# Optimization experiments

Measured on AMD Instinct MI355X. Metric: run time of the kernel, lower is better.

Reference implementation:

```python
import jax, jax.numpy as jnp
import numpy as np


def _gru_scan(x_seq, Wih, Whh, bih, bhh):
    # x_seq: (S, N, D); PyTorch GRU/GRUCell gate math, h0 = 0. Returns (S, N, H).
    H = Whh.shape[1]
    gi_all = x_seq @ Wih.T + bih  # precompute input projections: (S, N, 3H)

    def step(h, gi):
        gh = h @ Whh.T + bhh
        ir, iz, inn = jnp.split(gi, 3, axis=-1)
        hr, hz, hn = jnp.split(gh, 3, axis=-1)
        r = jax.nn.sigmoid(ir + hr)
        z = jax.nn.sigmoid(iz + hz)
        n = jnp.tanh(inn + r * hn)
        h_new = (1.0 - z) * n + z * h
        return h_new, h_new

    h0 = jnp.zeros((x_seq.shape[1], H), x_seq.dtype)
    _, ys = jax.lax.scan(step, h0, gi_all)
    return ys


def setup_inputs() -> dict:
    key = jax.random.key(0)
    ks = jax.random.split(key, 40)
    B, T = 32, 800
    NOTE, E, P, H0, H1, FE, RE = 128, 256, 256, 512, 512, 64, 64

    def w(k, shape):
        return jax.random.normal(k, shape, dtype=jnp.float32) * 0.05

    return {
        "note": jax.random.randint(ks[0], (B, T), 0, NOTE, dtype=jnp.int64),
        "f0_prev": jax.random.normal(ks[1], (B, T), dtype=jnp.float32),
        "rmse_prev": jax.random.normal(ks[2], (B, T), dtype=jnp.float32),
        "note_emb": w(ks[3], (NOTE, E)),
        "f0_W": w(ks[4], (FE, 1)), "f0_b": w(ks[5], (FE,)),
        "rmse_W": w(ks[6], (RE, 1)), "rmse_b": w(ks[7], (RE,)),
        "pre1_W": w(ks[8], (P, E)), "pre1_b": w(ks[9], (P,)),
        "pre2_W": w(ks[10], (P, P)), "pre2_b": w(ks[11], (P,)),
        "encf_Wih": w(ks[12], (3 * H0, P)), "encf_Whh": w(ks[13], (3 * H0, H0)),
        "encf_bih": w(ks[14], (3 * H0,)), "encf_bhh": w(ks[15], (3 * H0,)),
        "encb_Wih": w(ks[16], (3 * H0, P)), "encb_Whh": w(ks[17], (3 * H0, H0)),
        "encb_bih": w(ks[18], (3 * H0,)), "encb_bhh": w(ks[19], (3 * H0,)),
        "decf_Wih": w(ks[20], (3 * H1, 2 * H0 + FE)), "decf_Whh": w(ks[21], (3 * H1, H1)),
        "decf_bih": w(ks[22], (3 * H1,)), "decf_bhh": w(ks[23], (3 * H1,)),
        "decr_Wih": w(ks[24], (3 * H1, 2 * H0 + RE)), "decr_Whh": w(ks[25], (3 * H1, H1)),
        "decr_bih": w(ks[26], (3 * H1,)), "decr_bhh": w(ks[27], (3 * H1,)),
        "postf_W": w(ks[28], (1, H1)), "postf_b": w(ks[29], (1,)),
        "postr_W": w(ks[30], (1, H1)), "postr_b": w(ks[31], (1,)),
    }


def reference(note, f0_prev, rmse_prev, note_emb, f0_W, f0_b, rmse_W, rmse_b,
              pre1_W, pre1_b, pre2_W, pre2_b,
              encf_Wih, encf_Whh, encf_bih, encf_bhh,
              encb_Wih, encb_Whh, encb_bih, encb_bhh,
              decf_Wih, decf_Whh, decf_bih, decf_bhh,
              decr_Wih, decr_Whh, decr_bih, decr_bhh,
              postf_W, postf_b, postr_W, postr_b):
    # Embeddings. Linear(1, FE) on a [B,T] signal == outer-broadcast with W[:,0].
    ne = note_emb[note]                                   # (B, T, E)
    f0e = f0_prev[..., None] * f0_W[:, 0] + f0_b          # (B, T, FE)
    rme = rmse_prev[..., None] * rmse_W[:, 0] + rmse_b    # (B, T, RE)

    # Prenet: Linear -> Tanh -> Linear -> Tanh
    h = jnp.tanh(jnp.tanh(ne @ pre1_W.T + pre1_b) @ pre2_W.T + pre2_b)  # (B, T, P)

    # Encoder: torch nn.GRU built WITHOUT batch_first and called with lengths=None,
    # so the recurrence runs over axis 0 (B) with T acting as the GRU batch. Replicated.
    ef = _gru_scan(h, encf_Wih, encf_Whh, encf_bih, encf_bhh)            # (B, T, H0)
    eb = _gru_scan(h[::-1], encb_Wih, encb_Whh, encb_bih, encb_bhh)[::-1]
    enc = jnp.concatenate([ef, eb], axis=-1)                             # (B, T, 2H0)

    # Decoders: GRUCell loop over T with teacher forcing (y_prevs has T>1 steps),
    # so step-t input is concat(enc[:, t], embed(prev[:, t])) -> standard scan.
    xt = jnp.transpose(enc, (1, 0, 2))                                   # (T, B, 2H0)
    hf = _gru_scan(jnp.concatenate([xt, jnp.transpose(f0e, (1, 0, 2))], -1),
                   decf_Wih, decf_Whh, decf_bih, decf_bhh)               # (T, B, H1)
    hr = _gru_scan(jnp.concatenate([xt, jnp.transpose(rme, (1, 0, 2))], -1),
                   decr_Wih, decr_Whh, decr_bih, decr_bhh)               # (T, B, H1)

    f0 = jnp.transpose((hf @ postf_W.T + postf_b)[..., 0], (1, 0))       # (B, T)
    rmse = jnp.transpose((hr @ postr_W.T + postr_b)[..., 0], (1, 0))     # (B, T)
    return (f0, rmse)
```

## Files before the change

kernel.cpp:

```cpp
#include <hip/hip_runtime.h>
#include <hip/hip_bf16.h>


typedef __bf16 bf16;
typedef bf16 bf16x8 __attribute__((ext_vector_type(8)));
typedef float f32x4 __attribute__((ext_vector_type(4)));

#define BATCH 32
#define TLEN 800
#define BT (BATCH * TLEN)

__device__ __forceinline__ float bf2f(bf16 v) {
    unsigned short u = __builtin_bit_cast(unsigned short, v);
    unsigned int x = ((unsigned int)u) << 16;
    return __builtin_bit_cast(float, x);
}
__device__ __forceinline__ bf16 f2bf(float f) {
    unsigned int x = __builtin_bit_cast(unsigned int, f);
    unsigned int r = (x + 0x7FFFu + ((x >> 16) & 1u)) >> 16;
    return __builtin_bit_cast(bf16, (unsigned short)r);
}
__device__ __forceinline__ bf16x8 ld8f(const float* p) {
    f32x4 a = *(const f32x4*)p;
    f32x4 b = *(const f32x4*)(p + 4);
    bf16x8 r;
#pragma unroll
    for (int i = 0; i < 4; i++) {
        r[i] = f2bf(a[i]);
        r[i + 4] = f2bf(b[i]);
    }
    return r;
}
__device__ __forceinline__ void splitv(f32x4 a, f32x4 b, bf16x8& vh, bf16x8& vl) {
#pragma unroll
    for (int j = 0; j < 4; j++) {
        bf16 h0 = f2bf(a[j]);
        vh[j] = h0;
        vl[j] = f2bf(a[j] - bf2f(h0));
        bf16 h1 = f2bf(b[j]);
        vh[j + 4] = h1;
        vl[j + 4] = f2bf(b[j] - bf2f(h1));
    }
}
__device__ __forceinline__ f32x4 mfma16(bf16x8 a, bf16x8 b, f32x4 c) {
    return __builtin_amdgcn_mfma_f32_16x16x32_bf16(a, b, c, 0, 0, 0);
}
__device__ __forceinline__ float sigm(float x) { return 1.f / (1.f + __expf(-x)); }

template <int MODE>
__global__ __launch_bounds__(256) void gemm01_k(
    const int* __restrict__ note, const float* __restrict__ asrc,
    const float* __restrict__ W, const float* __restrict__ bias,
    float* __restrict__ out, int t0, int TC) {
    __shared__ bf16 Ah[128][72], Al[128][72], Bs[128][72];

    const int tid = threadIdx.x;
    const int lane = tid & 63, wv = tid >> 6;
    const int wm = wv & 1, wn = wv >> 1;
    const int l15 = lane & 15, hi = lane >> 4;
    const int bm = blockIdx.x * 128, bn = blockIdx.y * 128;
    const int ch = (tid & 7) * 8, arow = tid >> 3;

    f32x4 acc[4][4] = {};
    const float* ap[4];
    if (MODE == 0) {
        int zc = 0;
        for (int i = 0; i < 64; i++) zc += (note[2 * i + 1] == 0) ? 1 : 0;
        const bool n64 = (zc >= 60);
#pragma unroll
        for (int i = 0; i < 4; i++) {
            int m = bm + arow + 32 * i;
            int b = m / TC, tt = m - b * TC;
            int idx = b * TLEN + t0 + tt;
            int id = n64 ? note[2 * idx] : note[idx];
            id = id < 0 ? 0 : (id > 127 ? 127 : id);
            ap[i] = asrc + (size_t)id * 256;
        }
    } else {
#pragma unroll
        for (int i = 0; i < 4; i++) ap[i] = asrc + (size_t)(bm + arow + 32 * i) * 256;
    }

    for (int k0 = 0; k0 < 256; k0 += 64) {
#pragma unroll
        for (int i = 0; i < 4; i++) {
            int row = arow + 32 * i;
            f32x4 va = *(const f32x4*)(ap[i] + k0 + ch);
            f32x4 vb = *(const f32x4*)(ap[i] + k0 + ch + 4);
            bf16x8 vh, vl;
            splitv(va, vb, vh, vl);
            *(bf16x8*)&Ah[row][ch] = vh;
            *(bf16x8*)&Al[row][ch] = vl;
        }
#pragma unroll
        for (int i = 0; i < 4; i++) {
            int row = arow + 32 * i;
            *(bf16x8*)&Bs[row][ch] = ld8f(W + (size_t)(bn + row) * 256 + k0 + ch);
        }
        __syncthreads();
#pragma unroll
        for (int kk = 0; kk < 64; kk += 32) {
            bf16x8 ah[4], al[4], bb[4];
#pragma unroll
            for (int mt = 0; mt < 4; mt++) {
                ah[mt] = *(const bf16x8*)&Ah[wm * 64 + mt * 16 + l15][kk + hi * 8];
                al[mt] = *(const bf16x8*)&Al[wm * 64 + mt * 16 + l15][kk + hi * 8];
            }
#pragma unroll
            for (int nt = 0; nt < 4; nt++)
                bb[nt] = *(const bf16x8*)&Bs[wn * 64 + nt * 16 + l15][kk + hi * 8];
#pragma unroll
            for (int mt = 0; mt < 4; mt++)
#pragma unroll
                for (int nt = 0; nt < 4; nt++) {
                    acc[mt][nt] = mfma16(ah[mt], bb[nt], acc[mt][nt]);
                    acc[mt][nt] = mfma16(al[mt], bb[nt], acc[mt][nt]);
                }
        }
        __syncthreads();
    }

#pragma unroll
    for (int mt = 0; mt < 4; mt++)
#pragma unroll
        for (int nt = 0; nt < 4; nt++) {
            int n = bn + wn * 64 + nt * 16 + l15;
            float bs = bias[n];
#pragma unroll
            for (int r = 0; r < 4; r++) {
                int m = bm + wm * 64 + mt * 16 + hi * 4 + r;
                out[(size_t)m * 256 + n] = tanhf(acc[mt][nt][r] + bs);
            }
        }
}

__global__ __launch_bounds__(256) void gemm2_k(
    const float* __restrict__ ef, const float* __restrict__ eb,
    const float* __restrict__ sig, const float* __restrict__ sigW,
    const float* __restrict__ sigB, const float* __restrict__ W,
    const float* __restrict__ bias, float* __restrict__ out, int t0, int TC) {
    __shared__ bf16 Ah[128][72], Al[128][72];
    __shared__ bf16 Bh[64][72], Bl[64][72];

    const int tid = threadIdx.x;
    const int lane = tid & 63, wv = tid >> 6;
    const int wm = wv & 1, wn = wv >> 1;
    const int l15 = lane & 15, hi = lane >> 4;
    const int bm = blockIdx.x * 128, bn = blockIdx.y * 64;
    const int ch = (tid & 7) * 8, arow = tid >> 3;

    f32x4 acc[4][2] = {};
    int rb[4];
    float sigv[4];
#pragma unroll
    for (int i = 0; i < 4; i++) {
        int m = bm + arow + 32 * i;
        int tt = m >> 5, b = m & 31;
        rb[i] = b * TC + tt;
        sigv[i] = sig[b * TLEN + t0 + tt];
    }

    for (int k0 = 0; k0 < 1088; k0 += 64) {
#pragma unroll
        for (int i = 0; i < 4; i++) {
            int row = arow + 32 * i;
            int k = k0 + ch;
            f32x4 va, vb;
            if (k < 512) {
                va = *(const f32x4*)(ef + (size_t)rb[i] * 512 + k);
                vb = *(const f32x4*)(ef + (size_t)rb[i] * 512 + k + 4);
            } else if (k < 1024) {
                va = *(const f32x4*)(eb + (size_t)rb[i] * 512 + (k - 512));
                vb = *(const f32x4*)(eb + (size_t)rb[i] * 512 + (k - 512) + 4);
            } else {
                f32x4 w0 = *(const f32x4*)(sigW + ch);
                f32x4 w1 = *(const f32x4*)(sigW + ch + 4);
                f32x4 b0 = *(const f32x4*)(sigB + ch);
                f32x4 b1 = *(const f32x4*)(sigB + ch + 4);
                float s = sigv[i];
#pragma unroll
                for (int j = 0; j < 4; j++) {
                    va[j] = s * w0[j] + b0[j];
                    vb[j] = s * w1[j] + b1[j];
                }
            }
            bf16x8 vh, vl;
            splitv(va, vb, vh, vl);
            *(bf16x8*)&Ah[row][ch] = vh;
            *(bf16x8*)&Al[row][ch] = vl;
        }
#pragma unroll
        for (int i = 0; i < 2; i++) {
            int row = arow + 32 * i;
            const float* src = W + (size_t)(bn + row) * 1088 + k0 + ch;
            f32x4 va = *(const f32x4*)src;
            f32x4 vb = *(const f32x4*)(src + 4);
            bf16x8 vh, vl;
            splitv(va, vb, vh, vl);
            *(bf16x8*)&Bh[row][ch] = vh;
            *(bf16x8*)&Bl[row][ch] = vl;
        }
        __syncthreads();
#pragma unroll
        for (int kk = 0; kk < 64; kk += 32) {
            bf16x8 ah[4], al[4], bh[2], bl[2];
#pragma unroll
            for (int mt = 0; mt < 4; mt++) {
                ah[mt] = *(const bf16x8*)&Ah[wm * 64 + mt * 16 + l15][kk + hi * 8];
                al[mt] = *(const bf16x8*)&Al[wm * 64 + mt * 16 + l15][kk + hi * 8];
            }
#pragma unroll
            for (int nt = 0; nt < 2; nt++) {
                bh[nt] = *(const bf16x8*)&Bh[wn * 32 + nt * 16 + l15][kk + hi * 8];
                bl[nt] = *(const bf16x8*)&Bl[wn * 32 + nt * 16 + l15][kk + hi * 8];
            }
#pragma unroll
            for (int mt = 0; mt < 4; mt++)
#pragma unroll
                for (int nt = 0; nt < 2; nt++) {
                    acc[mt][nt] = mfma16(ah[mt], bh[nt], acc[mt][nt]);
                    acc[mt][nt] = mfma16(al[mt], bh[nt], acc[mt][nt]);
                    acc[mt][nt] = mfma16(ah[mt], bl[nt], acc[mt][nt]);
                }
        }
        __syncthreads();
    }

#pragma unroll
    for (int mt = 0; mt < 4; mt++)
#pragma unroll
        for (int nt = 0; nt < 2; nt++) {
            int n = bn + wn * 32 + nt * 16 + l15;
            float bs = bias[n];
#pragma unroll
            for (int r = 0; r < 4; r++) {
                int m = bm + wm * 64 + mt * 16 + hi * 4 + r;
                out[(size_t)m * 1536 + n] = acc[mt][nt][r] + bs;
            }
        }
}

__global__ __launch_bounds__(256) void enc_step_k(
    int step, int TC, const float* __restrict__ hpre, float* __restrict__ efb,
    float* __restrict__ ebb, const float* __restrict__ fWih,
    const float* __restrict__ fWhh, const float* __restrict__ fbih,
    const float* __restrict__ fbhh, const float* __restrict__ bWih,
    const float* __restrict__ bWhh, const float* __restrict__ bbih,
    const float* __restrict__ bbhh) {
    __shared__ bf16 As[32][72], Alo[32][72];
    __shared__ bf16 Bs[96][72], Blo[96][72];

    const int dir = blockIdx.z;
    const float* Wih = dir ? bWih : fWih;
    const float* Whh = dir ? bWhh : fWhh;
    const float* bih = dir ? bbih : fbih;
    const float* bhh = dir ? bbhh : fbhh;
    float* outb = dir ? ebb : efb;
    const int bsrc = dir ? (31 - step) : step;
    const int prevb = dir ? (32 - step) : (step - 1);

    const int tid = threadIdx.x;
    const int lane = tid & 63, wv = tid >> 6;
    const int mt = wv & 1, jt = wv >> 1;
    const int l15 = lane & 15, hi = lane >> 4;
    const int mtile = blockIdx.x, jtile = blockIdx.y;
    const int ch = (tid & 7) * 8, arow = tid >> 3;

    f32x4 acc_r = {}, acc_z = {}, acc_in = {}, acc_hn = {};

    const int nblocks = (step == 0) ? 4 : 12;
    for (int kb = 0; kb < nblocks; kb++) {
        int k0 = kb * 64;
        {
            int trow = mtile * 32 + arow;
            int tcl = trow < TC ? trow : TC - 1;
            const float* src = (k0 < 256)
                                   ? (hpre + ((size_t)bsrc * TC + tcl) * 256 + k0 + ch)
                                   : (outb + ((size_t)prevb * TC + tcl) * 512 + (k0 - 256) + ch);
            f32x4 va = *(const f32x4*)src;
            f32x4 vb = *(const f32x4*)(src + 4);
            bf16x8 vh, vl;
            splitv(va, vb, vh, vl);
            *(bf16x8*)&As[arow][ch] = vh;
            *(bf16x8*)&Alo[arow][ch] = vl;
        }
#pragma unroll
        for (int i = 0; i < 3; i++) {
            int row = arow + 32 * i;
            int s = row >> 5, j = row & 31;
            int wr = s * 512 + jtile * 32 + j;
            const float* src = (k0 < 256) ? (Wih + (size_t)wr * 256 + k0 + ch)
                                          : (Whh + (size_t)wr * 512 + (k0 - 256) + ch);
            f32x4 va = *(const f32x4*)src;
            f32x4 vb = *(const f32x4*)(src + 4);
            bf16x8 vh, vl;
            splitv(va, vb, vh, vl);
            *(bf16x8*)&Bs[row][ch] = vh;
            *(bf16x8*)&Blo[row][ch] = vl;
        }
        __syncthreads();
#pragma unroll
        for (int kk = 0; kk < 64; kk += 32) {
            bf16x8 a = *(const bf16x8*)&As[mt * 16 + l15][kk + hi * 8];
            bf16x8 alo = *(const bf16x8*)&Alo[mt * 16 + l15][kk + hi * 8];
            bf16x8 brh = *(const bf16x8*)&Bs[jt * 16 + l15][kk + hi * 8];
            bf16x8 brl = *(const bf16x8*)&Blo[jt * 16 + l15][kk + hi * 8];
            bf16x8 bzh = *(const bf16x8*)&Bs[32 + jt * 16 + l15][kk + hi * 8];
            bf16x8 bzl = *(const bf16x8*)&Blo[32 + jt * 16 + l15][kk + hi * 8];
            bf16x8 bnh = *(const bf16x8*)&Bs[64 + jt * 16 + l15][kk + hi * 8];
            bf16x8 bnl = *(const bf16x8*)&Blo[64 + jt * 16 + l15][kk + hi * 8];
            acc_r = mfma16(a, brh, acc_r);
            acc_r = mfma16(alo, brh, acc_r);
            acc_r = mfma16(a, brl, acc_r);
            acc_z = mfma16(a, bzh, acc_z);
            acc_z = mfma16(alo, bzh, acc_z);
            acc_z = mfma16(a, bzl, acc_z);
            if (k0 < 256) {
                acc_in = mfma16(a, bnh, acc_in);
                acc_in = mfma16(alo, bnh, acc_in);
                acc_in = mfma16(a, bnl, acc_in);
            } else {
                acc_hn = mfma16(a, bnh, acc_hn);
                acc_hn = mfma16(alo, bnh, acc_hn);
                acc_hn = mfma16(a, bnl, acc_hn);
            }
        }
        __syncthreads();
    }

    int j = jtile * 32 + jt * 16 + l15;
    float bir = bih[j] + bhh[j];
    float biz = bih[512 + j] + bhh[512 + j];
    float bin = bih[1024 + j];
    float bhn = bhh[1024 + j];
#pragma unroll
    for (int r = 0; r < 4; r++) {
        int trow = mtile * 32 + mt * 16 + hi * 4 + r;
        if (trow < TC) {
            float rr = sigm(acc_r[r] + bir);
            float zz = sigm(acc_z[r] + biz);
            float nn = tanhf(acc_in[r] + bin + rr * (acc_hn[r] + bhn));
            float hp = (step > 0) ? outb[((size_t)prevb * TC + trow) * 512 + j] : 0.f;
            outb[((size_t)bsrc * TC + trow) * 512 + j] = (1.f - zz) * nn + zz * hp;
        }
    }
}

__global__ __launch_bounds__(256, 1) void dec_k(
    const float* __restrict__ giF, const float* __restrict__ giR,
    const float* __restrict__ WhhF, const float* __restrict__ WhhR,
    const float* __restrict__ bhhF, const float* __restrict__ bhhR,
    float* __restrict__ HcurF, float* __restrict__ HcurR,
    const float* __restrict__ HprevF, const float* __restrict__ HprevR,
    int* __restrict__ flags, int t0, int TC) {
    const int d = blockIdx.x >> 4;
    const int g = blockIdx.x & 15;
    const float* gi = d ? giR : giF;
    const float* Whh = d ? WhhR : WhhF;
    const float* bhh = d ? bhhR : bhhF;
    float* Hcur = d ? HcurR : HcurF;
    const float* Hprev = d ? HprevR : HprevF;
    int* flg = flags + d * TLEN;

    const int tid = threadIdx.x;
    const int lane = tid & 63, wv = tid >> 6;
    const int mt = wv & 1, jt = wv >> 1;
    const int l15 = lane & 15, hi = lane >> 4;
    const int j_abs = g * 32 + jt * 16 + l15;

    bf16x8 Wf[3][16];
#pragma unroll
    for (int s = 0; s < 3; s++)
#pragma unroll
        for (int kb = 0; kb < 16; kb++)
            Wf[s][kb] = ld8f(Whh + (size_t)(s * 512 + j_abs) * 512 + kb * 32 + hi * 8);

    const float bhr = bhh[j_abs];
    const float bhz = bhh[512 + j_abs];
    const float bhn = bhh[1024 + j_abs];

    for (int tt = 0; tt < TC; tt++) {
        const int t = t0 + tt;
        float gr[4], gz[4], gn[4];
#pragma unroll
        for (int r = 0; r < 4; r++) {
            int b = mt * 16 + hi * 4 + r;
            const float* gp = gi + ((size_t)tt * BATCH + b) * 1536 + j_abs;
            gr[r] = gp[0];
            gz[r] = gp[512];
            gn[r] = gp[1024];
        }

        f32x4 ar = {}, az = {}, an = {};
        float hp[4] = {0.f, 0.f, 0.f, 0.f};
        if (t > 0) {
            const float* base;
            if (tt > 0) {
                if (tid == 0) {
                    while (__hip_atomic_load(&flg[t - 1], __ATOMIC_ACQUIRE,
                                             __HIP_MEMORY_SCOPE_AGENT) < 16)
                        __builtin_amdgcn_s_sleep(1);
                }
                __syncthreads();
                __threadfence();
                base = Hcur + (size_t)(tt - 1) * BATCH * 512;
            } else {
                base = Hprev + (size_t)(TC - 1) * BATCH * 512;
            }
            const float* ap = base + (size_t)(mt * 16 + l15) * 512 + hi * 8;
#pragma unroll
            for (int half = 0; half < 2; half++) {
                f32x4 raw[8][2];
#pragma unroll
                for (int q = 0; q < 8; q++) {
                    int kb = half * 8 + q;
                    raw[q][0] = *(const f32x4*)(ap + kb * 32);
                    raw[q][1] = *(const f32x4*)(ap + kb * 32 + 4);
                }
#pragma unroll
                for (int q = 0; q < 8; q++) {
                    int kb = half * 8 + q;
                    bf16x8 ah, al;
                    splitv(raw[q][0], raw[q][1], ah, al);
                    ar = mfma16(ah, Wf[0][kb], ar);
                    ar = mfma16(al, Wf[0][kb], ar);
                    az = mfma16(ah, Wf[1][kb], az);
                    az = mfma16(al, Wf[1][kb], az);
                    an = mfma16(ah, Wf[2][kb], an);
                    an = mfma16(al, Wf[2][kb], an);
                }
            }
#pragma unroll
            for (int r = 0; r < 4; r++) {
                int b = mt * 16 + hi * 4 + r;
                hp[r] = base[(size_t)b * 512 + j_abs];
            }
        }
#pragma unroll
        for (int r = 0; r < 4; r++) {
            int b = mt * 16 + hi * 4 + r;
            float rr = sigm(gr[r] + ar[r] + bhr);
            float zz = sigm(gz[r] + az[r] + bhz);
            float nn = tanhf(gn[r] + rr * (an[r] + bhn));
            Hcur[((size_t)tt * BATCH + b) * 512 + j_abs] = (1.f - zz) * nn + zz * hp[r];
        }
        __syncthreads();
        if (tid == 0)
            __hip_atomic_fetch_add(&flg[t], 1, __ATOMIC_RELEASE, __HIP_MEMORY_SCOPE_AGENT);
    }
}

__global__ __launch_bounds__(256) void post_k(
    const float* __restrict__ H, const float* __restrict__ W,
    const float* __restrict__ bs, float* __restrict__ out, int t0) {
    const int wv = threadIdx.x >> 6, lane = threadIdx.x & 63;
    const int row = blockIdx.x * 4 + wv;
    const int tt = row >> 5, b = row & 31;
    const float bias = bs[0];
    const float* hp = H + (size_t)row * 512 + lane * 8;
    f32x4 h0 = *(const f32x4*)hp;
    f32x4 h1 = *(const f32x4*)(hp + 4);
    f32x4 w0 = *(const f32x4*)(W + lane * 8);
    f32x4 w1 = *(const f32x4*)(W + lane * 8 + 4);
    float s = 0.f;
#pragma unroll
    for (int i = 0; i < 4; i++) s += h0[i] * w0[i] + h1[i] * w1[i];
#pragma unroll
    for (int off = 32; off > 0; off >>= 1) s += __shfl_down(s, off);
    if (lane == 0) out[b * TLEN + t0 + tt] = s + bias;
}

__global__ void zero_k(int* __restrict__ flags) {
    int i = blockIdx.x * 256 + threadIdx.x;
    if (i < 2 * TLEN) flags[i] = 0;
}

extern "C" void kernel_launch(void* const* d_in, const int* in_sizes, int n_in,
                              void* d_out, int out_size, void* d_ws, size_t ws_size,
                              hipStream_t stream) {
    const int* note = (const int*)d_in[0];
    const float* f0_prev = (const float*)d_in[1];
    const float* rmse_prev = (const float*)d_in[2];
    const float* note_emb = (const float*)d_in[3];
    const float* f0_W = (const float*)d_in[4];
    const float* f0_b = (const float*)d_in[5];
    const float* rmse_W = (const float*)d_in[6];
    const float* rmse_b = (const float*)d_in[7];
    const float* pre1_W = (const float*)d_in[8];
    const float* pre1_b = (const float*)d_in[9];
    const float* pre2_W = (const float*)d_in[10];
    const float* pre2_b = (const float*)d_in[11];
    const float* encf_Wih = (const float*)d_in[12];
    const float* encf_Whh = (const float*)d_in[13];
    const float* encf_bih = (const float*)d_in[14];
    const float* encf_bhh = (const float*)d_in[15];
    const float* encb_Wih = (const float*)d_in[16];
    const float* encb_Whh = (const float*)d_in[17];
    const float* encb_bih = (const float*)d_in[18];
    const float* encb_bhh = (const float*)d_in[19];
    const float* decf_Wih = (const float*)d_in[20];
    const float* decf_Whh = (const float*)d_in[21];
    const float* decf_bih = (const float*)d_in[22];
    const float* decf_bhh = (const float*)d_in[23];
    const float* decr_Wih = (const float*)d_in[24];
    const float* decr_Whh = (const float*)d_in[25];
    const float* decr_bih = (const float*)d_in[26];
    const float* decr_bhh = (const float*)d_in[27];
    const float* postf_W = (const float*)d_in[28];
    const float* postf_b = (const float*)d_in[29];
    const float* postr_W = (const float*)d_in[30];
    const float* postr_b = (const float*)d_in[31];
    float* out = (float*)d_out;

    const int tcs[9] = {800, 400, 200, 100, 80, 40, 20, 8, 4};
    int TC = 4;
    for (int i = 0; i < 9; i++) {
        int tc = tcs[i];
        int slots = (tc == TLEN) ? 1 : 2;
        size_t need = (size_t)(2 * 65536 + 2 * 196608 + 2 * slots * 65536) * tc + 65536;
        if (ws_size >= need) { TC = tc; break; }
    }
    const int NC = TLEN / TC;
    const int slots = (NC == 1) ? 1 : 2;

    char* ws = (char*)d_ws;
    size_t off = 0;
    auto carve = [&](size_t bytes) {
        void* p = ws + off;
        off += (bytes + 255) & ~(size_t)255;
        return p;
    };
    const size_t slotB = (size_t)65536 * TC;
    float* ef_c = (float*)carve(slotB);
    float* eb_c = (float*)carve(slotB);
    float* giF_c = (float*)carve((size_t)196608 * TC);
    float* giR_c = (float*)carve((size_t)196608 * TC);
    float* ringF = (float*)carve(slotB * slots);
    float* ringR = (float*)carve(slotB * slots);
    int* flags = (int*)carve(2 * TLEN * 4);
    float* t1_c = giF_c;
    float* hpre_c = giF_c + (size_t)8192 * TC;

    zero_k<<<dim3(7), 256, 0, stream>>>(flags);

    const size_t slotE = (size_t)TC * BATCH * 512;

    for (int c = 0; c < NC; c++) {
        const int t0 = c * TC;
        const int mg = TC * 32 / 128;

        gemm01_k<0><<<dim3(mg, 2), 256, 0, stream>>>(note, note_emb, pre1_W, pre1_b,
                                                     t1_c, t0, TC);
        gemm01_k<1><<<dim3(mg, 2), 256, 0, stream>>>(nullptr, t1_c, pre2_W, pre2_b,
                                                     hpre_c, t0, TC);
        const int etiles = (TC + 31) / 32;
        for (int i = 0; i < 32; i++)
            enc_step_k<<<dim3(etiles, 16, 2), 256, 0, stream>>>(
                i, TC, hpre_c, ef_c, eb_c, encf_Wih, encf_Whh, encf_bih, encf_bhh,
                encb_Wih, encb_Whh, encb_bih, encb_bhh);

        gemm2_k<<<dim3(mg, 24), 256, 0, stream>>>(ef_c, eb_c, f0_prev, f0_W, f0_b,
                                                  decf_Wih, decf_bih, giF_c, t0, TC);
        gemm2_k<<<dim3(mg, 24), 256, 0, stream>>>(ef_c, eb_c, rmse_prev, rmse_W,
                                                  rmse_b, decr_Wih, decr_bih, giR_c,
                                                  t0, TC);

        float* HcurF = ringF + (size_t)(c & (slots - 1)) * slotE;
        const float* HprevF = ringF + (size_t)((c - 1) & (slots - 1)) * slotE;
        float* HcurR = ringR + (size_t)(c & (slots - 1)) * slotE;
        const float* HprevR = ringR + (size_t)((c - 1) & (slots - 1)) * slotE;

        dec_k<<<dim3(32), 256, 0, stream>>>(giF_c, giR_c, decf_Whh, decr_Whh,
                                            decf_bhh, decr_bhh, HcurF, HcurR,
                                            HprevF, HprevR, flags, t0, TC);

        post_k<<<dim3(TC * 32 / 4), 256, 0, stream>>>(HcurF, postf_W, postf_b,
                                                      out, t0);
        post_k<<<dim3(TC * 32 / 4), 256, 0, stream>>>(HcurR, postr_W, postr_b,
                                                      out + BT, t0);
    }
    (void)in_sizes; (void)n_in; (void)out_size; (void)ws_size;
}
```

Measured before the change: 13.19 ms.

## Replace per-step counter barrier with per-block progress flags and relaxed coherent loads

The decoder's cross-block barrier changes from one atomic counter per timestep to one progress flag per block. Each block stores t+1 into its own flag, and 16 lanes of wave 0 poll all the flags in parallel. The acquire/release semantics and the explicit threadfence are dropped. Hidden-state stores and loads become relaxed agent-scope atomics, and the block's own previous h is kept in registers instead of being reloaded. The aim is to cut the latency of the per-step synchronisation in the serial 800-step recurrence. The cost is that correctness now relies on relaxed ordering behaving well on this hardware.

```diff
diff --git a/kernel.cpp b/kernel.cpp
--- a/kernel.cpp
+++ b/kernel.cpp
@@ -5,6 +5,7 @@
 typedef __bf16 bf16;
 typedef bf16 bf16x8 __attribute__((ext_vector_type(8)));
 typedef float f32x4 __attribute__((ext_vector_type(4)));
+typedef float f32x2 __attribute__((ext_vector_type(2)));
 
 #define BATCH 32
 #define TLEN 800
@@ -46,6 +47,29 @@
     return __builtin_amdgcn_mfma_f32_16x16x32_bf16(a, b, c, 0, 0, 0);
 }
 __device__ __forceinline__ float sigm(float x) { return 1.f / (1.f + __expf(-x)); }
+
+__device__ __forceinline__ void cst_f32(float* p, float v) {
+    __hip_atomic_store((unsigned int*)p, __builtin_bit_cast(unsigned int, v),
+                       __ATOMIC_RELAXED, __HIP_MEMORY_SCOPE_AGENT);
+}
+__device__ __forceinline__ float cld_f32(const float* p) {
+    unsigned int u = __hip_atomic_load((const unsigned int*)p, __ATOMIC_RELAXED,
+                                       __HIP_MEMORY_SCOPE_AGENT);
+    return __builtin_bit_cast(float, u);
+}
+__device__ __forceinline__ f32x4 cld_f32x4(const float* p) {
+    unsigned long long a = __hip_atomic_load((const unsigned long long*)p,
+                                             __ATOMIC_RELAXED,
+                                             __HIP_MEMORY_SCOPE_AGENT);
+    unsigned long long b = __hip_atomic_load((const unsigned long long*)(p + 2),
+                                             __ATOMIC_RELAXED,
+                                             __HIP_MEMORY_SCOPE_AGENT);
+    f32x2 fa = __builtin_bit_cast(f32x2, a);
+    f32x2 fb = __builtin_bit_cast(f32x2, b);
+    f32x4 r;
+    r[0] = fa[0]; r[1] = fa[1]; r[2] = fb[0]; r[3] = fb[1];
+    return r;
+}
 
 template <int MODE>
 __global__ __launch_bounds__(256) void gemm01_k(
@@ -360,7 +384,7 @@
     const float* bhh = d ? bhhR : bhhF;
     float* Hcur = d ? HcurR : HcurF;
     const float* Hprev = d ? HprevR : HprevF;
-    int* flg = flags + d * TLEN;
+    int* flg = flags + d * 16;
 
     const int tid = threadIdx.x;
     const int lane = tid & 63, wv = tid >> 6;
@@ -378,6 +402,8 @@
     const float bhr = bhh[j_abs];
     const float bhz = bhh[512 + j_abs];
     const float bhn = bhh[1024 + j_abs];
+
+    float hpreg[4] = {0.f, 0.f, 0.f, 0.f};
 
     for (int tt = 0; tt < TC; tt++) {
         const int t = t0 + tt;
@@ -396,13 +422,12 @@
         if (t > 0) {
             const float* base;
             if (tt > 0) {
-                if (tid == 0) {
-                    while (__hip_atomic_load(&flg[t - 1], __ATOMIC_ACQUIRE,
-                                             __HIP_MEMORY_SCOPE_AGENT) < 16)
+                if (wv == 0 && lane < 16) {
+                    while (__hip_atomic_load(&flg[lane], __ATOMIC_RELAXED,
+                                             __HIP_MEMORY_SCOPE_AGENT) < t)
                         __builtin_amdgcn_s_sleep(1);
                 }
                 __syncthreads();
-                __threadfence();
                 base = Hcur + (size_t)(tt - 1) * BATCH * 512;
             } else {
                 base = Hprev + (size_t)(TC - 1) * BATCH * 512;
@@ -414,8 +439,8 @@
 #pragma unroll
                 for (int q = 0; q < 8; q++) {
                     int kb = half * 8 + q;
-                    raw[q][0] = *(const f32x4*)(ap + kb * 32);
-                    raw[q][1] = *(const f32x4*)(ap + kb * 32 + 4);
+                    raw[q][0] = cld_f32x4(ap + kb * 32);
+                    raw[q][1] = cld_f32x4(ap + kb * 32 + 4);
                 }
 #pragma unroll
                 for (int q = 0; q < 8; q++) {
@@ -430,10 +455,15 @@
                     an = mfma16(al, Wf[2][kb], an);
                 }
             }
-#pragma unroll
-            for (int r = 0; r < 4; r++) {
-                int b = mt * 16 + hi * 4 + r;
-                hp[r] = base[(size_t)b * 512 + j_abs];
+            if (tt > 0) {
+#pragma unroll
+                for (int r = 0; r < 4; r++) hp[r] = hpreg[r];
+            } else {
+#pragma unroll
+                for (int r = 0; r < 4; r++) {
+                    int b = mt * 16 + hi * 4 + r;
+                    hp[r] = cld_f32(base + (size_t)b * 512 + j_abs);
+                }
             }
         }
 #pragma unroll
@@ -442,11 +472,14 @@
             float rr = sigm(gr[r] + ar[r] + bhr);
             float zz = sigm(gz[r] + az[r] + bhz);
             float nn = tanhf(gn[r] + rr * (an[r] + bhn));
-            Hcur[((size_t)tt * BATCH + b) * 512 + j_abs] = (1.f - zz) * nn + zz * hp[r];
+            float hnew = (1.f - zz) * nn + zz * hp[r];
+            cst_f32(&Hcur[((size_t)tt * BATCH + b) * 512 + j_abs], hnew);
+            hpreg[r] = hnew;
         }
         __syncthreads();
         if (tid == 0)
-            __hip_atomic_fetch_add(&flg[t], 1, __ATOMIC_RELEASE, __HIP_MEMORY_SCOPE_AGENT);
+            __hip_atomic_store(&flg[g], t + 1, __ATOMIC_RELAXED,
+                               __HIP_MEMORY_SCOPE_AGENT);
     }
 }
 
```

Result: faster. 12.00 ms (-9.0%).

## Use per-wave flag sync and packed bf16 hi/lo hidden state in decoder

Applied to the files above, without the earlier changes.

The decoder recurrence now stores each hidden value as a packed hi/lo bf16 pair in one u32, so consumers unpack with byte permutes instead of re-splitting fp32 values. The block-wide barrier and single-counter flag are replaced by per-wave monotonic step flags that every wave polls directly. The previous hidden value for the z*h term is also kept in registers rather than reloaded. This targets the cross-block synchronisation latency on the serial critical path. It relies on relaxed atomics plus acquire fences being enough for visibility, and the post kernel now reconstructs values from the packed pair.

```diff
diff --git a/kernel.cpp b/kernel.cpp
--- a/kernel.cpp
+++ b/kernel.cpp
@@ -5,6 +5,7 @@
 typedef __bf16 bf16;
 typedef bf16 bf16x8 __attribute__((ext_vector_type(8)));
 typedef float f32x4 __attribute__((ext_vector_type(4)));
+typedef unsigned int u32x4 __attribute__((ext_vector_type(4)));
 
 #define BATCH 32
 #define TLEN 800
@@ -46,6 +47,34 @@
     return __builtin_amdgcn_mfma_f32_16x16x32_bf16(a, b, c, 0, 0, 0);
 }
 __device__ __forceinline__ float sigm(float x) { return 1.f / (1.f + __expf(-x)); }
+
+__device__ __forceinline__ void cst_u32(unsigned int* p, unsigned int v) {
+    __hip_atomic_store(p, v, __ATOMIC_RELAXED, __HIP_MEMORY_SCOPE_AGENT);
+}
+__device__ __forceinline__ unsigned int cld_u32(const unsigned int* p) {
+    return __hip_atomic_load(p, __ATOMIC_RELAXED, __HIP_MEMORY_SCOPE_AGENT);
+}
+__device__ __forceinline__ unsigned long long cld_u64(const unsigned int* p) {
+    return __hip_atomic_load((const unsigned long long*)p, __ATOMIC_RELAXED,
+                             __HIP_MEMORY_SCOPE_AGENT);
+}
+__device__ __forceinline__ float pk2f(unsigned int pk) {
+    return bf2f(__builtin_bit_cast(bf16, (unsigned short)(pk >> 16))) +
+           bf2f(__builtin_bit_cast(bf16, (unsigned short)(pk & 0xFFFFu)));
+}
+__device__ __forceinline__ void unpk(const unsigned long long q[4], bf16x8& ah,
+                                     bf16x8& al) {
+    u32x4 hw, lw;
+#pragma unroll
+    for (int i = 0; i < 4; i++) {
+        unsigned int x = (unsigned int)q[i];
+        unsigned int y = (unsigned int)(q[i] >> 32);
+        hw[i] = __builtin_amdgcn_perm(y, x, 0x07060302u);
+        lw[i] = __builtin_amdgcn_perm(y, x, 0x05040100u);
+    }
+    ah = __builtin_bit_cast(bf16x8, hw);
+    al = __builtin_bit_cast(bf16x8, lw);
+}
 
 template <int MODE>
 __global__ __launch_bounds__(256) void gemm01_k(
@@ -350,23 +379,24 @@
     const float* __restrict__ giF, const float* __restrict__ giR,
     const float* __restrict__ WhhF, const float* __restrict__ WhhR,
     const float* __restrict__ bhhF, const float* __restrict__ bhhR,
-    float* __restrict__ HcurF, float* __restrict__ HcurR,
-    const float* __restrict__ HprevF, const float* __restrict__ HprevR,
+    unsigned int* __restrict__ HpkF, unsigned int* __restrict__ HpkR,
+    const unsigned int* __restrict__ HpvF, const unsigned int* __restrict__ HpvR,
     int* __restrict__ flags, int t0, int TC) {
     const int d = blockIdx.x >> 4;
     const int g = blockIdx.x & 15;
     const float* gi = d ? giR : giF;
     const float* Whh = d ? WhhR : WhhF;
     const float* bhh = d ? bhhR : bhhF;
-    float* Hcur = d ? HcurR : HcurF;
-    const float* Hprev = d ? HprevR : HprevF;
-    int* flg = flags + d * TLEN;
+    unsigned int* Hpk = d ? HpkR : HpkF;
+    const unsigned int* Hpv = d ? HpvR : HpvF;
+    int* flg = flags + d * 64;
 
     const int tid = threadIdx.x;
     const int lane = tid & 63, wv = tid >> 6;
     const int mt = wv & 1, jt = wv >> 1;
     const int l15 = lane & 15, hi = lane >> 4;
     const int j_abs = g * 32 + jt * 16 + l15;
+    const int wid = g * 4 + wv;
 
     bf16x8 Wf[3][16];
 #pragma unroll
@@ -378,6 +408,8 @@
     const float bhr = bhh[j_abs];
     const float bhz = bhh[512 + j_abs];
     const float bhn = bhh[1024 + j_abs];
+
+    float hpreg[4] = {0.f, 0.f, 0.f, 0.f};
 
     for (int tt = 0; tt < TC; tt++) {
         const int t = t0 + tt;
@@ -394,34 +426,34 @@
         f32x4 ar = {}, az = {}, an = {};
         float hp[4] = {0.f, 0.f, 0.f, 0.f};
         if (t > 0) {
-            const float* base;
+            const unsigned int* base;
             if (tt > 0) {
-                if (tid == 0) {
-                    while (__hip_atomic_load(&flg[t - 1], __ATOMIC_ACQUIRE,
-                                             __HIP_MEMORY_SCOPE_AGENT) < 16)
-                        __builtin_amdgcn_s_sleep(1);
+                while (true) {
+                    int v = __hip_atomic_load(&flg[lane], __ATOMIC_RELAXED,
+                                              __HIP_MEMORY_SCOPE_AGENT);
+                    if (!__any(v < t)) break;
+                    __builtin_amdgcn_s_sleep(1);
                 }
-                __syncthreads();
-                __threadfence();
-                base = Hcur + (size_t)(tt - 1) * BATCH * 512;
+                __builtin_amdgcn_fence(__ATOMIC_ACQUIRE, "agent");
+                base = Hpk + (size_t)(tt - 1) * BATCH * 512;
             } else {
-                base = Hprev + (size_t)(TC - 1) * BATCH * 512;
-            }
-            const float* ap = base + (size_t)(mt * 16 + l15) * 512 + hi * 8;
+                base = Hpv + (size_t)(TC - 1) * BATCH * 512;
+            }
+            const unsigned int* ap = base + (size_t)(mt * 16 + l15) * 512 + hi * 8;
 #pragma unroll
             for (int half = 0; half < 2; half++) {
-                f32x4 raw[8][2];
-#pragma unroll
-                for (int q = 0; q < 8; q++) {
-                    int kb = half * 8 + q;
-                    raw[q][0] = *(const f32x4*)(ap + kb * 32);
-                    raw[q][1] = *(const f32x4*)(ap + kb * 32 + 4);
+                unsigned long long q[8][4];
+#pragma unroll
+                for (int qq = 0; qq < 8; qq++) {
+                    const unsigned int* pp = ap + (half * 8 + qq) * 32;
+#pragma unroll
+                    for (int u = 0; u < 4; u++) q[qq][u] = cld_u64(pp + 2 * u);
                 }
 #pragma unroll
-                for (int q = 0; q < 8; q++) {
-                    int kb = half * 8 + q;
+                for (int qq = 0; qq < 8; qq++) {
+                    int kb = half * 8 + qq;
                     bf16x8 ah, al;
-                    splitv(raw[q][0], raw[q][1], ah, al);
+                    unpk(q[qq], ah, al);
                     ar = mfma16(ah, Wf[0][kb], ar);
                     ar = mfma16(al, Wf[0][kb], ar);
                     az = mfma16(ah, Wf[1][kb], az);
@@ -430,10 +462,15 @@
                     an = mfma16(al, Wf[2][kb], an);
                 }
             }
-#pragma unroll
-            for (int r = 0; r < 4; r++) {
-                int b = mt * 16 + hi * 4 + r;
-                hp[r] = base[(size_t)b * 512 + j_abs];
+            if (tt > 0) {
+#pragma unroll
+                for (int r = 0; r < 4; r++) hp[r] = hpreg[r];
+            } else {
+#pragma unroll
+                for (int r = 0; r < 4; r++) {
+                    int b = mt * 16 + hi * 4 + r;
+                    hp[r] = pk2f(cld_u32(base + (size_t)b * 512 + j_abs));
+                }
             }
         }
 #pragma unroll
@@ -442,29 +479,36 @@
             float rr = sigm(gr[r] + ar[r] + bhr);
             float zz = sigm(gz[r] + az[r] + bhz);
             float nn = tanhf(gn[r] + rr * (an[r] + bhn));
-            Hcur[((size_t)tt * BATCH + b) * 512 + j_abs] = (1.f - zz) * nn + zz * hp[r];
-        }
-        __syncthreads();
-        if (tid == 0)
-            __hip_atomic_fetch_add(&flg[t], 1, __ATOMIC_RELEASE, __HIP_MEMORY_SCOPE_AGENT);
+            float hnew = (1.f - zz) * nn + zz * hp[r];
+            bf16 hh = f2bf(hnew);
+            bf16 hl = f2bf(hnew - bf2f(hh));
+            unsigned int pk =
+                ((unsigned int)__builtin_bit_cast(unsigned short, hh) << 16) |
+                (unsigned int)__builtin_bit_cast(unsigned short, hl);
+            cst_u32(&Hpk[((size_t)tt * BATCH + b) * 512 + j_abs], pk);
+            hpreg[r] = hnew;
+        }
+        if (lane == 0)
+            __hip_atomic_store(&flg[wid], t + 1, __ATOMIC_RELEASE,
+                               __HIP_MEMORY_SCOPE_AGENT);
     }
 }
 
 __global__ __launch_bounds__(256) void post_k(
-    const float* __restrict__ H, const float* __restrict__ W,
+    const unsigned int* __restrict__ H, const float* __restrict__ W,
     const float* __restrict__ bs, float* __restrict__ out, int t0) {
     const int wv = threadIdx.x >> 6, lane = threadIdx.x & 63;
     const int row = blockIdx.x * 4 + wv;
     const int tt = row >> 5, b = row & 31;
     const float bias = bs[0];
-    const float* hp = H + (size_t)row * 512 + lane * 8;
-    f32x4 h0 = *(const f32x4*)hp;
-    f32x4 h1 = *(const f32x4*)(hp + 4);
+    const unsigned int* hp = H + (size_t)row * 512 + lane * 8;
+    u32x4 p0 = *(const u32x4*)hp;
+    u32x4 p1 = *(const u32x4*)(hp + 4);
     f32x4 w0 = *(const f32x4*)(W + lane * 8);
     f32x4 w1 = *(const f32x4*)(W + lane * 8 + 4);
     float s = 0.f;
 #pragma unroll
-    for (int i = 0; i < 4; i++) s += h0[i] * w0[i] + h1[i] * w1[i];
+    for (int i = 0; i < 4; i++) s += pk2f(p0[i]) * w0[i] + pk2f(p1[i]) * w1[i];
 #pragma unroll
     for (int off = 32; off > 0; off >>= 1) s += __shfl_down(s, off);
     if (lane == 0) out[b * TLEN + t0 + tt] = s + bias;
@@ -472,7 +516,9 @@
 
 __global__ void zero_k(int* __restrict__ flags) {
     int i = blockIdx.x * 256 + threadIdx.x;
-    if (i < 2 * TLEN) flags[i] = 0;
+    if (i < 2 * TLEN)
+        __hip_atomic_store(&flags[i], 0, __ATOMIC_RELAXED,
+                           __HIP_MEMORY_SCOPE_AGENT);
 }
 
 extern "C" void kernel_launch(void* const* d_in, const int* in_sizes, int n_in,
@@ -535,8 +581,8 @@
     float* eb_c = (float*)carve(slotB);
     float* giF_c = (float*)carve((size_t)196608 * TC);
     float* giR_c = (float*)carve((size_t)196608 * TC);
-    float* ringF = (float*)carve(slotB * slots);
-    float* ringR = (float*)carve(slotB * slots);
+    unsigned int* ringF = (unsigned int*)carve(slotB * slots);
+    unsigned int* ringR = (unsigned int*)carve(slotB * slots);
     int* flags = (int*)carve(2 * TLEN * 4);
     float* t1_c = giF_c;
     float* hpre_c = giF_c + (size_t)8192 * TC;
@@ -565,10 +611,10 @@
                                                   rmse_b, decr_Wih, decr_bih, giR_c,
                                                   t0, TC);
 
-        float* HcurF = ringF + (size_t)(c & (slots - 1)) * slotE;
-        const float* HprevF = ringF + (size_t)((c - 1) & (slots - 1)) * slotE;
-        float* HcurR = ringR + (size_t)(c & (slots - 1)) * slotE;
-        const float* HprevR = ringR + (size_t)((c - 1) & (slots - 1)) * slotE;
+        unsigned int* HcurF = ringF + (size_t)(c & (slots - 1)) * slotE;
+        const unsigned int* HprevF = ringF + (size_t)((c - 1) & (slots - 1)) * slotE;
+        unsigned int* HcurR = ringR + (size_t)(c & (slots - 1)) * slotE;
+        const unsigned int* HprevR = ringR + (size_t)((c - 1) & (slots - 1)) * slotE;
 
         dec_k<<<dim3(32), 256, 0, stream>>>(giF_c, giR_c, decf_Whh, decr_Whh,
                                             decf_bhh, decr_bhh, HcurF, HcurR,
```

New measurement: 15.57 ms. 18.1% more time.
